# Performance work log

Measured on AMD Instinct MI355X. Metric: run time of the kernel, lower is better.

The kernel has to match this reference:

```python
import jax, jax.numpy as jnp
import numpy as np

B, SQ, SK, D, H, DH = 4, 1024, 1024, 1024, 16, 64

def setup_inputs() -> dict:
    key = jax.random.key(0)
    ks = jax.random.split(key, 7)
    s = 0.02
    return {
        "input_ids": jax.random.normal(ks[0], (B, SQ, D), jnp.float32),
        "encoder_output": jax.random.normal(ks[1], (B, SK, D), jnp.float32),
        "position_bias": jax.random.normal(ks[2], (1, H, SQ, SK), jnp.float32),
        "Wq": jax.random.normal(ks[3], (D, H * DH), jnp.float32) * s,
        "Wk": jax.random.normal(ks[4], (D, H * DH), jnp.float32) * s,
        "Wv": jax.random.normal(ks[5], (D, H * DH), jnp.float32) * s,
        "Wo": jax.random.normal(ks[6], (H * DH, D), jnp.float32) * s,
    }

def reference(input_ids, encoder_output, position_bias, Wq, Wk, Wv, Wo):
    # bias-free projections (nn.Linear(..., bias=False))
    q = (input_ids @ Wq).reshape(B, SQ, H, DH).transpose(0, 2, 1, 3)      # [B,H,Sq,dh]
    k = (encoder_output @ Wk).reshape(B, SK, H, DH).transpose(0, 2, 1, 3)  # [B,H,Sk,dh]
    v = (encoder_output @ Wv).reshape(B, SK, H, DH).transpose(0, 2, 1, 3)  # [B,H,Sk,dh]
    # T5-style attention: NO 1/sqrt(dh) scaling, additive position bias
    scores = jnp.einsum("bhqd,bhkd->bhqk", q, k) + position_bias          # [B,H,Sq,Sk]
    attn = jax.nn.softmax(scores, axis=-1)
    ctx = jnp.einsum("bhqk,bhkd->bhqd", attn, v)                          # [B,H,Sq,dh]
    ctx = ctx.transpose(0, 2, 1, 3).reshape(B, SQ, H * DH)
    return ctx @ Wo                                                        # [B,Sq,D]
```

## Files before the change

kernel.cpp:

```cpp
#include <hip/hip_runtime.h>

typedef _Float16 f16;
typedef _Float16 f16x4 __attribute__((ext_vector_type(4)));
typedef _Float16 f16x8 __attribute__((ext_vector_type(8)));
typedef float f32x4 __attribute__((ext_vector_type(4)));

#define LOADLDS16(gp, lp)                                                     \
  __builtin_amdgcn_global_load_lds(                                           \
      (const __attribute__((address_space(1))) void*)(gp),                    \
      (__attribute__((address_space(3))) void*)(lp), 16, 0, 0)

__global__ __launch_bounds__(256) void k_cast(const float* __restrict__ x,
                                              f16* __restrict__ y, int n4) {
  int i = blockIdx.x * 256 + threadIdx.x;
  if (i >= n4) return;
  float4 v = reinterpret_cast<const float4*>(x)[i];
  f16x4 o;
  o[0] = (f16)v.x; o[1] = (f16)v.y; o[2] = (f16)v.z; o[3] = (f16)v.w;
  reinterpret_cast<f16x4*>(y)[i] = o;
}

__global__ __launch_bounds__(256) void k_castw_t(
    const float* __restrict__ w0, const float* __restrict__ w1,
    const float* __restrict__ w2, const float* __restrict__ w3,
    f16* __restrict__ o0, f16* __restrict__ o1, f16* __restrict__ o2,
    f16* __restrict__ o3) {
  const float* W;
  f16* O;
  switch (blockIdx.z) {
    case 0: W = w0; O = o0; break;
    case 1: W = w1; O = o1; break;
    case 2: W = w2; O = o2; break;
    default: W = w3; O = o3; break;
  }
  __shared__ f16 T[64][72];
  const int tid = threadIdx.x;
  const int r0 = blockIdx.y * 64, c0 = blockIdx.x * 64;
#pragma unroll
  for (int i = 0; i < 4; ++i) {
    int c = i * 256 + tid;
    int row = c >> 4, col = (c & 15) * 4;
    float4 v = *reinterpret_cast<const float4*>(W + (size_t)(r0 + row) * 1024 + c0 + col);
    T[col + 0][row] = (f16)v.x;
    T[col + 1][row] = (f16)v.y;
    T[col + 2][row] = (f16)v.z;
    T[col + 3][row] = (f16)v.w;
  }
  __syncthreads();
#pragma unroll
  for (int i = 0; i < 2; ++i) {
    int c = i * 256 + tid;
    int cc = c >> 3, ro = (c & 7) * 8;
    f16x8 v;
#pragma unroll
    for (int j = 0; j < 8; ++j) v[j] = T[cc][ro + j];
    *reinterpret_cast<f16x8*>(O + (size_t)(c0 + cc) * 1024 + r0 + ro) = v;
  }
}

__global__ __launch_bounds__(256) void k_gemm_qkv(const f16* __restrict__ Xq,
                                                  const f16* __restrict__ Xkv,
                                                  const f16* __restrict__ Bt,
                                                  f16* __restrict__ outp) {
  __shared__ f16 As[128 * 64];
  __shared__ f16 Bs[128 * 64];
  const int tid = threadIdx.x;
  const int w = tid >> 6, l = tid & 63;
  const int lr = l & 15, lq = l >> 4;
  const int m0 = blockIdx.y * 128, n0 = blockIdx.x * 128;
  const f16* A = (n0 < 1024) ? Xq : Xkv;
  const int wr = (w >> 1) * 64, wc = (w & 1) * 64;
  const int K = 1024;
  f32x4 acc[4][4] = {};
  for (int kt = 0; kt < K; kt += 64) {
#pragma unroll
    for (int i = 0; i < 4; ++i) {
      int c = (i * 4 + w) * 64 + l;
      LOADLDS16(A + (size_t)(m0 + (c >> 3)) * K + kt + (c & 7) * 8,
                As + (size_t)(i * 4 + w) * 512);
      LOADLDS16(Bt + (size_t)(n0 + (c >> 3)) * K + kt + (c & 7) * 8,
                Bs + (size_t)(i * 4 + w) * 512);
    }
    __syncthreads();
#pragma unroll
    for (int kk = 0; kk < 2; ++kk) {
      f16x8 af[4], bf[4];
#pragma unroll
      for (int m = 0; m < 4; ++m)
        af[m] = *reinterpret_cast<const f16x8*>(As + (wr + m * 16 + lr) * 64 + kk * 32 + lq * 8);
#pragma unroll
      for (int n = 0; n < 4; ++n)
        bf[n] = *reinterpret_cast<const f16x8*>(Bs + (wc + n * 16 + lr) * 64 + kk * 32 + lq * 8);
#pragma unroll
      for (int m = 0; m < 4; ++m)
#pragma unroll
        for (int n = 0; n < 4; ++n)
          acc[m][n] = __builtin_amdgcn_mfma_f32_16x16x32_f16(af[m], bf[n], acc[m][n], 0, 0, 0);
    }
    __syncthreads();
  }
#pragma unroll
  for (int m = 0; m < 4; ++m)
#pragma unroll
    for (int n = 0; n < 4; ++n)
#pragma unroll
      for (int r = 0; r < 4; ++r) {
        int row = m0 + wr + m * 16 + lq * 4 + r;
        int col = n0 + wc + n * 16 + lr;
        int b = row >> 10, s = row & 1023;
        int plane = col >> 10, cc = col & 1023;
        int h = cc >> 6, dh = cc & 63;
        outp[(size_t)plane * 4194304 +
             (((size_t)(b * 16 + h)) * 1024 + s) * 64 + dh] = (f16)acc[m][n][r];
      }
}

__global__ __launch_bounds__(256) void k_gemm_o(const f16* __restrict__ A,
                                                const f16* __restrict__ Bt,
                                                float* __restrict__ out, int M,
                                                int N, int K) {
  __shared__ f16 As[64 * 64];
  __shared__ f16 Bs[128 * 64];
  const int tid = threadIdx.x;
  const int w = tid >> 6, l = tid & 63;
  const int lr = l & 15, lq = l >> 4;
  const int m0 = blockIdx.y * 64, n0 = blockIdx.x * 128;
  const int wr = (w >> 1) * 32, wc = (w & 1) * 64;
  f32x4 acc[2][4] = {};
  for (int kt = 0; kt < K; kt += 64) {
#pragma unroll
    for (int i = 0; i < 2; ++i) {
      int c = (i * 4 + w) * 64 + l;
      LOADLDS16(A + (size_t)(m0 + (c >> 3)) * K + kt + (c & 7) * 8,
                As + (size_t)(i * 4 + w) * 512);
    }
#pragma unroll
    for (int i = 0; i < 4; ++i) {
      int c = (i * 4 + w) * 64 + l;
      LOADLDS16(Bt + (size_t)(n0 + (c >> 3)) * K + kt + (c & 7) * 8,
                Bs + (size_t)(i * 4 + w) * 512);
    }
    __syncthreads();
#pragma unroll
    for (int kk = 0; kk < 2; ++kk) {
      f16x8 af[2], bf[4];
#pragma unroll
      for (int m = 0; m < 2; ++m)
        af[m] = *reinterpret_cast<const f16x8*>(As + (wr + m * 16 + lr) * 64 + kk * 32 + lq * 8);
#pragma unroll
      for (int n = 0; n < 4; ++n)
        bf[n] = *reinterpret_cast<const f16x8*>(Bs + (wc + n * 16 + lr) * 64 + kk * 32 + lq * 8);
#pragma unroll
      for (int m = 0; m < 2; ++m)
#pragma unroll
        for (int n = 0; n < 4; ++n)
          acc[m][n] = __builtin_amdgcn_mfma_f32_16x16x32_f16(af[m], bf[n], acc[m][n], 0, 0, 0);
    }
    __syncthreads();
  }
#pragma unroll
  for (int m = 0; m < 2; ++m)
#pragma unroll
    for (int n = 0; n < 4; ++n)
#pragma unroll
      for (int r = 0; r < 4; ++r) {
        int row = m0 + wr + m * 16 + lq * 4 + r;
        int col = n0 + wc + n * 16 + lr;
        out[(size_t)row * N + col] = acc[m][n][r];
      }
}

__global__ __launch_bounds__(256) void k_vtrans(const f16* __restrict__ vb,
                                                f16* __restrict__ vtb) {
  const int bh = blockIdx.y, s0 = blockIdx.x * 64;
  __shared__ f16 T[64][72];
  const int tid = threadIdx.x;
  const f16* src = vb + (size_t)bh * 1024 * 64;
#pragma unroll
  for (int i = 0; i < 2; ++i) {
    int c = i * 256 + tid;
    int row = c >> 3, co = (c & 7) * 8;
    f16x8 v = *reinterpret_cast<const f16x8*>(src + (size_t)(s0 + row) * 64 + co);
#pragma unroll
    for (int j = 0; j < 8; ++j) T[co + j][row] = v[j];
  }
  __syncthreads();
  f16* dst = vtb + (size_t)bh * 64 * 1024;
#pragma unroll
  for (int i = 0; i < 2; ++i) {
    int c = i * 256 + tid;
    int dh = c >> 3, so = (c & 7) * 8;
    f16x8 v;
#pragma unroll
    for (int j = 0; j < 8; ++j) v[j] = T[dh][so + j];
    *reinterpret_cast<f16x8*>(dst + (size_t)dh * 1024 + s0 + so) = v;
  }
}

__global__ __launch_bounds__(256) void k_attn(const f16* __restrict__ qb,
                                              const f16* __restrict__ kb,
                                              const f16* __restrict__ vtb,
                                              const float* __restrict__ bias,
                                              f16* __restrict__ ctx) {
  const int bid = blockIdx.x;
  const int ord = (bid & 7) * 128 + (bid >> 3);
  const int h = ord >> 6, qt = (ord >> 2) & 15, b = ord & 3;
  const int bh = b * 16 + h;
  const int q0 = qt * 64;
  const int tid = threadIdx.x, w = tid >> 6, l = tid & 63;
  const int lr = l & 15, lq = l >> 4;

  __shared__ f16 Kb[2][2048];
  __shared__ f16 Vb[2][2048];
  __shared__ float Bbf[2][2048];
  __shared__ f16 Ps[4][640];

  const f16* qp = qb + ((size_t)bh * 1024 + q0 + w * 16 + lr) * 64 + lq * 8;
  f16x8 qf0 = *reinterpret_cast<const f16x8*>(qp);
  f16x8 qf1 = *reinterpret_cast<const f16x8*>(qp + 32);

  f32x4 O[4] = {};
  float mrun[4], rsum[4];
#pragma unroll
  for (int r = 0; r < 4; ++r) { mrun[r] = -3.0e38f; rsum[r] = 0.f; }

  const f16* kbase = kb + (size_t)bh * 1024 * 64;
  const f16* vbase = vtb + (size_t)bh * 64 * 1024;
  const float* bbase = bias + ((size_t)h * 1024 + q0) * 1024;

  const int krow = w * 8 + (l >> 3);
  const int kg = (l & 7) ^ (l >> 3);
  const int vrow = w * 16 + (l >> 2);
  const int vg = (l & 3) ^ ((l >> 3) & 3);
  const int brow = w * 16 + (l >> 3);
  const int bgs = (l & 7) ^ ((l >> 3) & 7);

  auto stage = [&](int t, int nxt) {
    LOADLDS16(kbase + (size_t)(t * 32 + krow) * 64 + kg * 8, &Kb[nxt][w * 512]);
    LOADLDS16(vbase + (size_t)vrow * 1024 + t * 32 + vg * 8, &Vb[nxt][w * 512]);
    LOADLDS16(bbase + (size_t)brow * 1024 + t * 32 + bgs * 4, &Bbf[nxt][w * 512]);
    LOADLDS16(bbase + (size_t)(brow + 8) * 1024 + t * 32 + bgs * 4,
              &Bbf[nxt][w * 512 + 256]);
  };

  stage(0, 0);
  __syncthreads();

#pragma unroll 1
  for (int t = 0; t < 32; ++t) {
    const int cur = t & 1;
    if (t < 31) stage(t + 1, cur ^ 1);
    __builtin_amdgcn_sched_barrier(0);

    f32x4 S[2] = {};
    __builtin_amdgcn_s_setprio(1);
#pragma unroll
    for (int c = 0; c < 2; ++c) {
      int row = c * 16 + lr;
      const f16* kbp = &Kb[cur][row * 64];
      f16x8 kf0 = *reinterpret_cast<const f16x8*>(kbp + ((lq ^ (lr & 7)) * 8));
      f16x8 kf1 = *reinterpret_cast<const f16x8*>(kbp + (((4 + lq) ^ (lr & 7)) * 8));
      S[c] = __builtin_amdgcn_mfma_f32_16x16x32_f16(qf0, kf0, S[c], 0, 0, 0);
      S[c] = __builtin_amdgcn_mfma_f32_16x16x32_f16(qf1, kf1, S[c], 0, 0, 0);
    }
    __builtin_amdgcn_s_setprio(0);

#pragma unroll
    for (int c = 0; c < 2; ++c)
#pragma unroll
      for (int r = 0; r < 4; ++r) {
        int row = w * 16 + lq * 4 + r;
        int G = c * 4 + (lr >> 2);
        S[c][r] += Bbf[cur][row * 32 + ((G ^ (row & 7)) << 2) + (lr & 3)];
      }

    float tmax[4];
#pragma unroll
    for (int r = 0; r < 4; ++r) tmax[r] = fmaxf(S[0][r], S[1][r]);
    bool ok = true;
#pragma unroll
    for (int r = 0; r < 4; ++r) ok = ok && (tmax[r] <= mrun[r] + 8.0f);
    if (!__all(ok)) {
#pragma unroll
      for (int msk = 1; msk <= 8; msk <<= 1)
#pragma unroll
        for (int r = 0; r < 4; ++r)
          tmax[r] = fmaxf(tmax[r], __shfl_xor(tmax[r], msk, 64));
#pragma unroll
      for (int r = 0; r < 4; ++r) {
        float mnew = fmaxf(mrun[r], tmax[r]);
        float sc = __expf(mrun[r] - mnew);
        mrun[r] = mnew;
        rsum[r] *= sc;
#pragma unroll
        for (int c = 0; c < 4; ++c) O[c][r] *= sc;
      }
    }

#pragma unroll
    for (int c = 0; c < 2; ++c)
#pragma unroll
      for (int r = 0; r < 4; ++r) {
        float p = __expf(S[c][r] - mrun[r]);
        rsum[r] += p;
        Ps[w][(lq * 4 + r) * 40 + c * 16 + lr] = (f16)p;
      }

    {
      f16x8 pa = *reinterpret_cast<const f16x8*>(&Ps[w][lr * 40 + lq * 8]);
      __builtin_amdgcn_s_setprio(1);
#pragma unroll
      for (int c = 0; c < 4; ++c) {
        int row = c * 16 + lr;
        f16x8 vf = *reinterpret_cast<const f16x8*>(
            &Vb[cur][row * 32 + ((lq ^ ((lr >> 1) & 3)) * 8)]);
        O[c] = __builtin_amdgcn_mfma_f32_16x16x32_f16(pa, vf, O[c], 0, 0, 0);
      }
      __builtin_amdgcn_s_setprio(0);
    }

    __syncthreads();
  }

#pragma unroll
  for (int msk = 1; msk <= 8; msk <<= 1)
#pragma unroll
    for (int r = 0; r < 4; ++r) rsum[r] += __shfl_xor(rsum[r], msk, 64);

#pragma unroll
  for (int c = 0; c < 4; ++c)
#pragma unroll
    for (int r = 0; r < 4; ++r) {
      float o = O[c][r] / rsum[r];
      int row = q0 + w * 16 + lq * 4 + r;
      ctx[((size_t)b * 1024 + row) * 1024 + h * 64 + c * 16 + lr] = (f16)o;
    }
}

extern "C" void kernel_launch(void* const* d_in, const int* in_sizes, int n_in,
                              void* d_out, int out_size, void* d_ws,
                              size_t ws_size, hipStream_t stream) {
  const float* input_ids = (const float*)d_in[0];
  const float* enc = (const float*)d_in[1];
  const float* bias = (const float*)d_in[2];
  const float* Wq = (const float*)d_in[3];
  const float* Wk = (const float*)d_in[4];
  const float* Wv = (const float*)d_in[5];
  const float* Wo = (const float*)d_in[6];

  char* ws = (char*)d_ws;
  const size_t MB = 1024 * 1024;
  f16* Xq  = (f16*)(ws + 0 * MB);
  f16* Xkv = (f16*)(ws + 8 * MB);
  f16* Wqt = (f16*)(ws + 16 * MB);
  f16* Wkt = (f16*)(ws + 18 * MB);
  f16* Wvt = (f16*)(ws + 20 * MB);
  f16* Wot = (f16*)(ws + 22 * MB);
  f16* qbuf = (f16*)(ws + 24 * MB);
  f16* kbuf = (f16*)(ws + 32 * MB);
  f16* vbuf = (f16*)(ws + 40 * MB);
  f16* vtb = Xkv;
  f16* ctxb = Xq;

  k_cast<<<4096, 256, 0, stream>>>(input_ids, Xq, 1048576);
  k_cast<<<4096, 256, 0, stream>>>(enc, Xkv, 1048576);
  k_castw_t<<<dim3(16, 16, 4), 256, 0, stream>>>(Wq, Wk, Wv, Wo, Wqt, Wkt, Wvt, Wot);

  k_gemm_qkv<<<dim3(24, 32), 256, 0, stream>>>(Xq, Xkv, Wqt, qbuf);

  k_vtrans<<<dim3(16, 64), 256, 0, stream>>>(vbuf, vtb);

  k_attn<<<1024, 256, 0, stream>>>(qbuf, kbuf, vtb, bias, ctxb);

  k_gemm_o<<<dim3(8, 64), 256, 0, stream>>>(ctxb, Wot, (float*)d_out, 4096, 1024, 1024);
}
```

Before: 150.0 us.

## Transpose QK^T MFMA so each lane owns a query row; merge input casts

Swaps the MFMA operand order so each lane holds scores for a single query row. That lets the bias be preloaded as one vector LDS read into the accumulator, and turns the row max and sum into scalars needing two shuffles instead of four per row. The P tile is written as packed f16x4 stores. Rescale factors and final sums are redistributed to the O layout with shuffles. The two activation cast launches are merged into one kernel to save a launch.

Measured after the change: 140.1 us. -6.6%, faster.

```diff
diff --git a/kernel.cpp b/kernel.cpp
--- a/kernel.cpp
+++ b/kernel.cpp
@@ -10,10 +10,18 @@
       (const __attribute__((address_space(1))) void*)(gp),                    \
       (__attribute__((address_space(3))) void*)(lp), 16, 0, 0)
 
-__global__ __launch_bounds__(256) void k_cast(const float* __restrict__ x,
-                                              f16* __restrict__ y, int n4) {
+__global__ __launch_bounds__(256) void k_cast2(const float* __restrict__ a,
+                                               const float* __restrict__ b,
+                                               f16* __restrict__ ya,
+                                               f16* __restrict__ yb) {
   int i = blockIdx.x * 256 + threadIdx.x;
-  if (i >= n4) return;
+  const float* x;
+  f16* y;
+  if (i < 1048576) {
+    x = a; y = ya;
+  } else {
+    x = b; y = yb; i -= 1048576;
+  }
   float4 v = reinterpret_cast<const float4*>(x)[i];
   f16x4 o;
   o[0] = (f16)v.x; o[1] = (f16)v.y; o[2] = (f16)v.z; o[3] = (f16)v.w;
@@ -220,9 +228,7 @@
   f16x8 qf1 = *reinterpret_cast<const f16x8*>(qp + 32);
 
   f32x4 O[4] = {};
-  float mrun[4], rsum[4];
-#pragma unroll
-  for (int r = 0; r < 4; ++r) { mrun[r] = -3.0e38f; rsum[r] = 0.f; }
+  float mrun = -3.0e38f, rsum = 0.f;
 
   const f16* kbase = kb + (size_t)bh * 1024 * 64;
   const f16* vbase = vtb + (size_t)bh * 64 * 1024;
@@ -252,7 +258,14 @@
     if (t < 31) stage(t + 1, cur ^ 1);
     __builtin_amdgcn_sched_barrier(0);
 
-    f32x4 S[2] = {};
+    f32x4 S[2];
+#pragma unroll
+    for (int c = 0; c < 2; ++c) {
+      int G = c * 4 + lq;
+      S[c] = *reinterpret_cast<const f32x4*>(
+          &Bbf[cur][(w * 16 + lr) * 32 + ((G ^ (lr & 7)) << 2)]);
+    }
+
     __builtin_amdgcn_s_setprio(1);
 #pragma unroll
     for (int c = 0; c < 2; ++c) {
@@ -260,51 +273,38 @@
       const f16* kbp = &Kb[cur][row * 64];
       f16x8 kf0 = *reinterpret_cast<const f16x8*>(kbp + ((lq ^ (lr & 7)) * 8));
       f16x8 kf1 = *reinterpret_cast<const f16x8*>(kbp + (((4 + lq) ^ (lr & 7)) * 8));
-      S[c] = __builtin_amdgcn_mfma_f32_16x16x32_f16(qf0, kf0, S[c], 0, 0, 0);
-      S[c] = __builtin_amdgcn_mfma_f32_16x16x32_f16(qf1, kf1, S[c], 0, 0, 0);
+      S[c] = __builtin_amdgcn_mfma_f32_16x16x32_f16(kf0, qf0, S[c], 0, 0, 0);
+      S[c] = __builtin_amdgcn_mfma_f32_16x16x32_f16(kf1, qf1, S[c], 0, 0, 0);
     }
     __builtin_amdgcn_s_setprio(0);
 
-#pragma unroll
-    for (int c = 0; c < 2; ++c)
+    float tmax = fmaxf(fmaxf(fmaxf(S[0][0], S[0][1]), fmaxf(S[0][2], S[0][3])),
+                       fmaxf(fmaxf(S[1][0], S[1][1]), fmaxf(S[1][2], S[1][3])));
+    if (!__all(tmax <= mrun + 8.0f)) {
+      tmax = fmaxf(tmax, __shfl_xor(tmax, 16, 64));
+      tmax = fmaxf(tmax, __shfl_xor(tmax, 32, 64));
+      float mnew = fmaxf(mrun, tmax);
+      float sc = __expf(mrun - mnew);
+      mrun = mnew;
+      rsum *= sc;
+      int sb = l & 48;
 #pragma unroll
       for (int r = 0; r < 4; ++r) {
-        int row = w * 16 + lq * 4 + r;
-        int G = c * 4 + (lr >> 2);
-        S[c][r] += Bbf[cur][row * 32 + ((G ^ (row & 7)) << 2) + (lr & 3)];
+        float scO = __shfl(sc, sb | (lq * 4 + r), 64);
+#pragma unroll
+        for (int c = 0; c < 4; ++c) O[c][r] *= scO;
       }
-
-    float tmax[4];
-#pragma unroll
-    for (int r = 0; r < 4; ++r) tmax[r] = fmaxf(S[0][r], S[1][r]);
-    bool ok = true;
-#pragma unroll
-    for (int r = 0; r < 4; ++r) ok = ok && (tmax[r] <= mrun[r] + 8.0f);
-    if (!__all(ok)) {
-#pragma unroll
-      for (int msk = 1; msk <= 8; msk <<= 1)
-#pragma unroll
-        for (int r = 0; r < 4; ++r)
-          tmax[r] = fmaxf(tmax[r], __shfl_xor(tmax[r], msk, 64));
-#pragma unroll
-      for (int r = 0; r < 4; ++r) {
-        float mnew = fmaxf(mrun[r], tmax[r]);
-        float sc = __expf(mrun[r] - mnew);
-        mrun[r] = mnew;
-        rsum[r] *= sc;
-#pragma unroll
-        for (int c = 0; c < 4; ++c) O[c][r] *= sc;
-      }
-    }
-
-#pragma unroll
-    for (int c = 0; c < 2; ++c)
-#pragma unroll
-      for (int r = 0; r < 4; ++r) {
-        float p = __expf(S[c][r] - mrun[r]);
-        rsum[r] += p;
-        Ps[w][(lq * 4 + r) * 40 + c * 16 + lr] = (f16)p;
-      }
+    }
+
+#pragma unroll
+    for (int c = 0; c < 2; ++c) {
+      f32x4 p;
+#pragma unroll
+      for (int r = 0; r < 4; ++r) p[r] = __expf(S[c][r] - mrun);
+      rsum += (p[0] + p[1]) + (p[2] + p[3]);
+      f16x4 ph = {(f16)p[0], (f16)p[1], (f16)p[2], (f16)p[3]};
+      *reinterpret_cast<f16x4*>(&Ps[w][lr * 40 + c * 16 + lq * 4]) = ph;
+    }
 
     {
       f16x8 pa = *reinterpret_cast<const f16x8*>(&Ps[w][lr * 40 + lq * 8]);
@@ -322,16 +322,18 @@
     __syncthreads();
   }
 
-#pragma unroll
-  for (int msk = 1; msk <= 8; msk <<= 1)
-#pragma unroll
-    for (int r = 0; r < 4; ++r) rsum[r] += __shfl_xor(rsum[r], msk, 64);
+  rsum += __shfl_xor(rsum, 16, 64);
+  rsum += __shfl_xor(rsum, 32, 64);
+  int sb = l & 48;
+  float rs[4];
+#pragma unroll
+  for (int r = 0; r < 4; ++r) rs[r] = __shfl(rsum, sb | (lq * 4 + r), 64);
 
 #pragma unroll
   for (int c = 0; c < 4; ++c)
 #pragma unroll
     for (int r = 0; r < 4; ++r) {
-      float o = O[c][r] / rsum[r];
+      float o = O[c][r] / rs[r];
       int row = q0 + w * 16 + lq * 4 + r;
       ctx[((size_t)b * 1024 + row) * 1024 + h * 64 + c * 16 + lr] = (f16)o;
     }
@@ -362,8 +364,7 @@
   f16* vtb = Xkv;
   f16* ctxb = Xq;
 
-  k_cast<<<4096, 256, 0, stream>>>(input_ids, Xq, 1048576);
-  k_cast<<<4096, 256, 0, stream>>>(enc, Xkv, 1048576);
+  k_cast2<<<8192, 256, 0, stream>>>(input_ids, enc, Xq, Xkv);
   k_castw_t<<<dim3(16, 16, 4), 256, 0, stream>>>(Wq, Wk, Wv, Wo, Wqt, Wkt, Wvt, Wot);
 
   k_gemm_qkv<<<dim3(24, 32), 256, 0, stream>>>(Xq, Xkv, Wqt, qbuf);
```
